# Performance work log

Hardware: AMD Instinct MI355X
Metric: run time of the kernel (lower is better)

The kernel has to match this reference:

```python
import jax, jax.numpy as jnp
import numpy as np

S = 41          # seq_len
D_IN = 1280
D_OUT = 1024
HEADS = 4
HC = D_OUT // HEADS
EPS = 1e-5

# ---- static edge construction (faithful to the torch code, incl. duplicate edges) ----

def _local_edges(s, window=1):
    e = []
    for i in range(s):
        for j in range(max(0, i - window), min(s, i + window + 1)):
            if i != j:
                e += [(i, j), (j, i)]
    return np.array(e, dtype=np.int32).T

def _region_edges(s):
    e = []
    step = s // 3
    for st in range(0, s, step):
        blk = range(st, min(st + step, s))
        for i in blk:
            for j in blk:
                if i != j:
                    e += [(i, j), (j, i)]
    return np.array(e, dtype=np.int32).T

def _global_edges(s):
    r, c = np.triu_indices(s, 1)  # torch.combinations: (i, j) with i < j
    return np.stack([r, c]).astype(np.int32)

def _batch_edges(e, b, s):
    off = np.arange(b, dtype=np.int32) * s
    return (e[:, None, :] + off[None, :, None]).reshape(2, -1)

_LOCAL = _local_edges(S)
_REGION = _region_edges(S)
_GLOBAL = _global_edges(S)

# ---- layer primitives ----

def _layernorm(x, g, b):
    mu = x.mean(-1, keepdims=True)
    v = ((x - mu) ** 2).mean(-1, keepdims=True)
    return (x - mu) / jnp.sqrt(v + EPS) * g + b

def _gcn(x, w, b, src, tgt, n):
    # PyG GCNConv: x' = D^-1/2 (A + I) D^-1/2 (x W) + b
    h = x @ w
    sl = jnp.arange(n, dtype=src.dtype)
    s = jnp.concatenate([src, sl]); t = jnp.concatenate([tgt, sl])
    deg = jax.ops.segment_sum(jnp.ones(t.shape, h.dtype), t, n)
    dinv = jnp.where(deg > 0, jax.lax.rsqrt(jnp.maximum(deg, 1.0)), 0.0)
    norm = dinv[s] * dinv[t]
    return jax.ops.segment_sum(h[s] * norm[:, None], t, n) + b

def _gat(x, w, a_src, a_dst, b, src, tgt, n):
    # PyG GATConv (shared lin, self loops, leaky_relu 0.2, softmax over incoming edges)
    h = (x @ w).reshape(n, HEADS, HC)
    sl = jnp.arange(n, dtype=src.dtype)
    s = jnp.concatenate([src, sl]); t = jnp.concatenate([tgt, sl])
    al_s = (h * a_src).sum(-1)  # [n, H]
    al_d = (h * a_dst).sum(-1)
    e = jax.nn.leaky_relu(al_s[s] + al_d[t], 0.2)  # [E, H]
    m = jax.ops.segment_max(e, t, n)
    ex = jnp.exp(e - m[t])
    den = jax.ops.segment_sum(ex, t, n)
    alpha = ex / den[t]
    out = jax.ops.segment_sum(h[s] * alpha[:, :, None], t, n)
    return out.reshape(n, HEADS * HC) + b

def _sage(x, wl, bl, wr, src, tgt, n):
    # PyG SAGEConv: mean-aggregate neighbors, plus root transform
    cnt = jax.ops.segment_sum(jnp.ones(src.shape, x.dtype), tgt, n)
    agg = jax.ops.segment_sum(x[src], tgt, n) / jnp.maximum(cnt, 1.0)[:, None]
    return agg @ wl + bl + x @ wr


def setup_inputs() -> dict:
    key = jax.random.key(0)
    ks = jax.random.split(key, 16)
    sc = 0.02
    f32 = jnp.float32
    inp = {
        'x': jax.random.normal(ks[0], (512, S, D_IN), f32),
        'att_w': jax.random.normal(ks[1], (D_IN, 1), f32) * sc,
        'att_b': jnp.zeros((1,), f32),
        'gcn_w': jax.random.normal(ks[2], (D_IN, D_OUT), f32) * sc,
        'gcn_b': jnp.zeros((D_OUT,), f32),
        'sn_g': jnp.ones((D_OUT,), f32), 'sn_b': jnp.zeros((D_OUT,), f32),
        'gat_w': jax.random.normal(ks[3], (D_IN, D_OUT), f32) * sc,
        'gat_as': jax.random.normal(ks[4], (HEADS, HC), f32) * sc,
        'gat_ad': jax.random.normal(ks[5], (HEADS, HC), f32) * sc,
        'gat_b': jnp.zeros((D_OUT,), f32),
        'mn_g': jnp.ones((D_OUT,), f32), 'mn_b': jnp.zeros((D_OUT,), f32),
        'sage_wl': jax.random.normal(ks[6], (D_IN, D_OUT), f32) * sc,
        'sage_bl': jnp.zeros((D_OUT,), f32),
        'sage_wr': jax.random.normal(ks[7], (D_IN, D_OUT), f32) * sc,
        'fp_w1': jax.random.normal(ks[8], (D_IN, 512), f32) * sc,
        'fp_b1': jnp.zeros((512,), f32),
        'fp_w2': jax.random.normal(ks[9], (512, S), f32) * sc,
        'fp_b2': jnp.zeros((S,), f32),
        'dn_g': jnp.ones((D_OUT,), f32), 'dn_b': jnp.zeros((D_OUT,), f32),
        'gate_w': jax.random.normal(ks[10], (3 * D_OUT, 3), f32) * sc,
        'gate_b': jnp.zeros((3,), f32),
    }
    return inp


def reference(x, att_w, att_b, gcn_w, gcn_b, sn_g, sn_b, gat_w, gat_as, gat_ad, gat_b,
              mn_g, mn_b, sage_wl, sage_bl, sage_wr, fp_w1, fp_b1, fp_w2, fp_b2,
              dn_g, dn_b, gate_w, gate_b):
    B = x.shape[0]
    N = B * S
    le = jnp.asarray(_batch_edges(_LOCAL, B, S))
    re = jnp.asarray(_batch_edges(_REGION, B, S))
    ge = jnp.asarray(_batch_edges(_GLOBAL, B, S))

    xf = x.reshape(N, D_IN)
    # shallow: local gating -> GCN -> LN
    enhanced = xf * jax.nn.sigmoid(xf @ att_w + att_b)
    shallow = _gcn(enhanced, gcn_w, gcn_b, le[0], le[1], N)
    shallow = _layernorm(shallow.reshape(B, S, D_OUT), sn_g, sn_b)
    # medium: GAT over region blocks -> LN
    gat = _gat(xf, gat_w, gat_as[None], gat_ad[None], gat_b, re[0], re[1], N)
    gat = _layernorm(gat.reshape(B, S, D_OUT), mn_g, mn_b)
    # deep: learned propagation mixing, SAGE over global edges -> LN
    pw = jax.nn.softmax(jax.nn.relu(x @ fp_w1 + fp_b1) @ fp_w2 + fp_b2, axis=-1)  # [B,S,S]
    sage_in = jnp.einsum('bij,bjd->bid', pw, x).reshape(N, D_IN)
    sage = _sage(sage_in, sage_wl, sage_bl, sage_wr, ge[0], ge[1], N)
    sage = _layernorm(sage.reshape(B, S, D_OUT), dn_g, dn_b)
    # gated branch mixing
    combined = jnp.concatenate([shallow, gat, sage], axis=-1)
    gates = jax.nn.softmax(combined @ gate_w + gate_b, axis=-1)
    total = gates[..., 0:1] * shallow + gates[..., 1:2] * gat + gates[..., 2:3] * sage
    return (shallow, gat, total)
```

## Files before the change

### kernel.cpp

```cpp
#include <hip/hip_runtime.h>
#include <math.h>

static constexpr int S    = 41;
static constexpr int DIN  = 1280;
static constexpr int DOUT = 1024;
static constexpr int HEADS = 4;
static constexpr int HC   = 256;

typedef __attribute__((ext_vector_type(4))) float f32x4;
typedef __attribute__((ext_vector_type(8))) short short8;

__device__ __forceinline__ ushort f2bf(float f) {
  uint u = __float_as_uint(f);
  uint r = u + 0x7fffu + ((u >> 16) & 1u);
  return (ushort)(r >> 16);
}
__device__ __forceinline__ float bf2f(ushort u) {
  return __uint_as_float(((uint)u) << 16);
}

__device__ __forceinline__ void gload16(const ushort* g, ushort* l) {
  __builtin_amdgcn_global_load_lds((const __attribute__((address_space(1))) void*)g,
                                   (__attribute__((address_space(3))) void*)l, 16, 0, 0);
}


__device__ __forceinline__ float warpReduceSum(float v) {
#pragma unroll
  for (int off = 32; off; off >>= 1) v += __shfl_down(v, off);
  return v;
}

__device__ __forceinline__ void blockReduce6(float* v) {
  __shared__ float red6[6][4];
  int w = threadIdx.x >> 6, lane = threadIdx.x & 63;
#pragma unroll
  for (int r = 0; r < 6; ++r) v[r] = warpReduceSum(v[r]);
  __syncthreads();
  if (lane == 0) {
#pragma unroll
    for (int r = 0; r < 6; ++r) red6[r][w] = v[r];
  }
  __syncthreads();
#pragma unroll
  for (int r = 0; r < 6; ++r)
    v[r] = red6[r][0] + red6[r][1] + red6[r][2] + red6[r][3];
}

__device__ __forceinline__ void blockReduce3v(float* v) {
  __shared__ float red3[3][4];
  int w = threadIdx.x >> 6, lane = threadIdx.x & 63;
#pragma unroll
  for (int r = 0; r < 3; ++r) v[r] = warpReduceSum(v[r]);
  __syncthreads();
  if (lane == 0) {
#pragma unroll
    for (int r = 0; r < 3; ++r) red3[r][w] = v[r];
  }
  __syncthreads();
#pragma unroll
  for (int r = 0; r < 3; ++r)
    v[r] = red3[r][0] + red3[r][1] + red3[r][2] + red3[r][3];
}


__global__ __launch_bounds__(256) void cvtsig_kernel(
    const float4* __restrict__ x, const float* __restrict__ att_w,
    const float* __restrict__ att_b, ushort4* __restrict__ xb, float* __restrict__ sig)
{
  int row  = blockIdx.x * 4 + (threadIdx.x >> 6);
  int lane = threadIdx.x & 63;
  const float4* xr = x + (size_t)row * (DIN / 4);
  const float4* wr = (const float4*)att_w;
  ushort4* xo = xb + (size_t)row * (DIN / 4);
  float acc = 0.f;
#pragma unroll
  for (int k = 0; k < DIN / 4 / 64; ++k) {
    float4 a = xr[lane + k * 64];
    float4 w = wr[lane + k * 64];
    acc += a.x * w.x + a.y * w.y + a.z * w.z + a.w * w.w;
    ushort4 o;
    o.x = f2bf(a.x); o.y = f2bf(a.y); o.z = f2bf(a.z); o.w = f2bf(a.w);
    xo[lane + k * 64] = o;
  }
  acc = warpReduceSum(acc);
  if (lane == 0) sig[row] = 1.f / (1.f + expf(-(acc + att_b[0])));
}


__global__ __launch_bounds__(256) void wcvt_kernel(const float* __restrict__ W,
                                                   ushort* __restrict__ out,
                                                   int K, int N, int ostride, int koff) {
  __shared__ float t[32][33];
  int n0 = blockIdx.x * 32, k0 = blockIdx.y * 32;
  int tx = threadIdx.x & 31, ty = threadIdx.x >> 5;
#pragma unroll
  for (int r = 0; r < 4; ++r) {
    int k = ty + r * 8;
    t[k][tx] = W[(size_t)(k0 + k) * N + n0 + tx];
  }
  __syncthreads();
#pragma unroll
  for (int r = 0; r < 4; ++r) {
    int nn = ty + r * 8;
    out[(size_t)(n0 + nn) * ostride + koff + k0 + tx] = f2bf(t[tx][nn]);
  }
}

__global__ __launch_bounds__(256) void w2cvt_kernel(const float* __restrict__ w2,
                                                    ushort* __restrict__ wpw) {
  int idx = blockIdx.x * 256 + threadIdx.x;
  int n = idx >> 9, k = idx & 511;
  wpw[idx] = (n < S) ? f2bf(w2[(size_t)k * S + n]) : (ushort)0;
}


struct Epi {
  void* dst[5];
  const float* bias[5];
  int nend[5];
  int ld[5];
  int relu[5];
  const float* rs;
};


__global__ __launch_bounds__(512, 1) void gemm256(
    const ushort* __restrict__ A, const ushort* __restrict__ Bt, int K, int nb, Epi e)
{
  __shared__ __align__(16) ushort As[3][256 * 32];
  __shared__ __align__(16) ushort Bs[3][256 * 32];

  const int bid = blockIdx.x;
  const int bm  = (bid / nb) * 256;
  const int bn  = (bid % nb) * 256;

  const int tid  = threadIdx.x;
  const int w    = tid >> 6;
  const int lane = tid & 63;
  const int l16  = lane & 15;
  const int l4   = lane >> 4;
  const int wr   = w >> 2;
  const int wc   = w & 3;
  const int m0   = wr * 128;
  const int n0   = wc * 64;

  const int rloc = lane >> 2;
  const int cpos = lane & 3;
  const int cdat = (cpos - (rloc >> 1)) & 3;
  const int srow = w * 32 + rloc;
  const int scol = cdat * 8;

  f32x4 acc[8][4];
#pragma unroll
  for (int i = 0; i < 8; ++i)
#pragma unroll
    for (int j = 0; j < 4; ++j) acc[i][j] = (f32x4)0.f;

  const ushort* pA0 = A  + (size_t)(bm + srow) * K + scol;
  const ushort* pA1 = A  + (size_t)(bm + srow + 16) * K + scol;
  const ushort* pB0 = Bt + (size_t)(bn + srow) * K + scol;
  const ushort* pB1 = Bt + (size_t)(bn + srow + 16) * K + scol;

  auto stage = [&](int buf, int kt) {
    gload16(pA0 + kt, &As[buf][w * 1024]);
    gload16(pA1 + kt, &As[buf][w * 1024 + 512]);
    gload16(pB0 + kt, &Bs[buf][w * 1024]);
    gload16(pB1 + kt, &Bs[buf][w * 1024 + 512]);
  };

  const int rchunk = ((l4 + (l16 >> 1)) & 3) * 8;

  const int nsteps = K >> 5;
  stage(0, 0); stage(1, 32); stage(2, 64);

  for (int t = 0; t < nsteps; ++t) {
    if (t == 0)                asm volatile("s_waitcnt vmcnt(8)" ::: "memory");
    else if (t == nsteps - 1)  asm volatile("s_waitcnt vmcnt(0)" ::: "memory");
    else                       asm volatile("s_waitcnt vmcnt(4)" ::: "memory");
    __builtin_amdgcn_s_barrier();
    asm volatile("" ::: "memory");

    if (t >= 1 && t + 2 < nsteps) stage((t + 2) % 3, (t + 2) * 32);

    const int cur = t % 3;
    short8 a[8], b[4];
#pragma unroll
    for (int i = 0; i < 8; ++i)
      a[i] = *reinterpret_cast<const short8*>(&As[cur][(m0 + i * 16 + l16) * 32 + rchunk]);
#pragma unroll
    for (int j = 0; j < 4; ++j)
      b[j] = *reinterpret_cast<const short8*>(&Bs[cur][(n0 + j * 16 + l16) * 32 + rchunk]);
    __builtin_amdgcn_s_setprio(1);
#pragma unroll
    for (int i = 0; i < 8; ++i)
#pragma unroll
      for (int j = 0; j < 4; ++j)
        acc[i][j] = __builtin_amdgcn_mfma_f32_16x16x32_bf16(a[i], b[j], acc[i][j], 0, 0, 0);
    __builtin_amdgcn_s_setprio(0);
  }

  void* dstv; const float* bias; const float* rs = nullptr; int ldc, cb, relu;
  if (bn < e.nend[0])      { dstv = e.dst[0]; ldc = e.ld[0]; cb = bn;             bias = e.bias[0]; relu = e.relu[0]; rs = e.rs; }
  else if (bn < e.nend[1]) { dstv = e.dst[1]; ldc = e.ld[1]; cb = bn - e.nend[0]; bias = e.bias[1]; relu = e.relu[1]; }
  else if (bn < e.nend[2]) { dstv = e.dst[2]; ldc = e.ld[2]; cb = bn - e.nend[1]; bias = e.bias[2]; relu = e.relu[2]; }
  else if (bn < e.nend[3]) { dstv = e.dst[3]; ldc = e.ld[3]; cb = bn - e.nend[2]; bias = e.bias[3]; relu = e.relu[3]; }
  else                     { dstv = e.dst[4]; ldc = e.ld[4]; cb = bn - e.nend[3]; bias = e.bias[4]; relu = e.relu[4]; }

#pragma unroll
  for (int i = 0; i < 8; ++i) {
    int mbase = bm + m0 + i * 16 + l4 * 4;
    float rsv[4];
#pragma unroll
    for (int r = 0; r < 4; ++r) rsv[r] = rs ? rs[mbase + r] : 1.f;
#pragma unroll
    for (int j = 0; j < 4; ++j) {
      int col = cb + n0 + j * 16 + l16;
      float bv = bias ? bias[col] : 0.f;
#pragma unroll
      for (int r = 0; r < 4; ++r) {
        float t = acc[i][j][r] * rsv[r] + bv;
        if (relu) t = fmaxf(t, 0.f);
        ((ushort*)dstv)[(size_t)(mbase + r) * ldc + col] = f2bf(t);
      }
    }
  }
}


template<bool F32OUT>
__global__ __launch_bounds__(256) void gemm_bf16(
    const ushort* __restrict__ A, const ushort* __restrict__ Bt, int K, int nb, Epi e)
{
  __shared__ __align__(16) ushort As[3][128 * 32];
  __shared__ __align__(16) ushort Bs[3][128 * 32];

  const int bid = blockIdx.x;
  const int bm  = (bid / nb) * 128;
  const int bn  = (bid % nb) * 128;

  const int tid  = threadIdx.x;
  const int w    = tid >> 6;
  const int lane = tid & 63;
  const int l16  = lane & 15;
  const int l4   = lane >> 4;
  const int m0   = (w >> 1) * 64;
  const int n0   = (w & 1) * 64;

  const int rloc = lane >> 2;
  const int cpos = lane & 3;
  const int cdat = (cpos - (rloc >> 1)) & 3;
  const int srow = w * 32 + rloc;
  const int scol = cdat * 8;

  f32x4 acc[4][4];
#pragma unroll
  for (int i = 0; i < 4; ++i)
#pragma unroll
    for (int j = 0; j < 4; ++j) acc[i][j] = (f32x4)0.f;

  const ushort* pA0 = A  + (size_t)(bm + srow) * K + scol;
  const ushort* pA1 = A  + (size_t)(bm + srow + 16) * K + scol;
  const ushort* pB0 = Bt + (size_t)(bn + srow) * K + scol;
  const ushort* pB1 = Bt + (size_t)(bn + srow + 16) * K + scol;

  auto stage = [&](int buf, int kt) {
    gload16(pA0 + kt, &As[buf][w * 1024]);
    gload16(pA1 + kt, &As[buf][w * 1024 + 512]);
    gload16(pB0 + kt, &Bs[buf][w * 1024]);
    gload16(pB1 + kt, &Bs[buf][w * 1024 + 512]);
  };

  const int rchunk = ((l4 + (l16 >> 1)) & 3) * 8;

  const int nsteps = K >> 5;
  stage(0, 0); stage(1, 32); stage(2, 64);

  for (int t = 0; t < nsteps; ++t) {
    if (t == 0)                asm volatile("s_waitcnt vmcnt(8)" ::: "memory");
    else if (t == nsteps - 1)  asm volatile("s_waitcnt vmcnt(0)" ::: "memory");
    else                       asm volatile("s_waitcnt vmcnt(4)" ::: "memory");
    __builtin_amdgcn_s_barrier();
    asm volatile("" ::: "memory");

    if (t >= 1 && t + 2 < nsteps) stage((t + 2) % 3, (t + 2) * 32);

    const int cur = t % 3;
    short8 a[4], b[4];
#pragma unroll
    for (int i = 0; i < 4; ++i)
      a[i] = *reinterpret_cast<const short8*>(&As[cur][(m0 + i * 16 + l16) * 32 + rchunk]);
#pragma unroll
    for (int j = 0; j < 4; ++j)
      b[j] = *reinterpret_cast<const short8*>(&Bs[cur][(n0 + j * 16 + l16) * 32 + rchunk]);
    __builtin_amdgcn_s_setprio(1);
#pragma unroll
    for (int i = 0; i < 4; ++i)
#pragma unroll
      for (int j = 0; j < 4; ++j)
        acc[i][j] = __builtin_amdgcn_mfma_f32_16x16x32_bf16(a[i], b[j], acc[i][j], 0, 0, 0);
    __builtin_amdgcn_s_setprio(0);
  }

  void* dstv; const float* bias; const float* rs = nullptr; int ldc, cb, relu;
  if (bn < e.nend[0])      { dstv = e.dst[0]; ldc = e.ld[0]; cb = bn;             bias = e.bias[0]; relu = e.relu[0]; rs = e.rs; }
  else if (bn < e.nend[1]) { dstv = e.dst[1]; ldc = e.ld[1]; cb = bn - e.nend[0]; bias = e.bias[1]; relu = e.relu[1]; }
  else if (bn < e.nend[2]) { dstv = e.dst[2]; ldc = e.ld[2]; cb = bn - e.nend[1]; bias = e.bias[2]; relu = e.relu[2]; }
  else if (bn < e.nend[3]) { dstv = e.dst[3]; ldc = e.ld[3]; cb = bn - e.nend[2]; bias = e.bias[3]; relu = e.relu[3]; }
  else                     { dstv = e.dst[4]; ldc = e.ld[4]; cb = bn - e.nend[3]; bias = e.bias[4]; relu = e.relu[4]; }

#pragma unroll
  for (int i = 0; i < 4; ++i) {
    int mbase = bm + m0 + i * 16 + l4 * 4;
    float rsv[4];
#pragma unroll
    for (int r = 0; r < 4; ++r) rsv[r] = rs ? rs[mbase + r] : 1.f;
#pragma unroll
    for (int j = 0; j < 4; ++j) {
      int col = cb + n0 + j * 16 + l16;
      float bv = bias ? bias[col] : 0.f;
#pragma unroll
      for (int r = 0; r < 4; ++r) {
        float t = acc[i][j][r] * rsv[r] + bv;
        if (relu) t = fmaxf(t, 0.f);
        if (F32OUT) ((float*)dstv)[(size_t)(mbase + r) * ldc + col] = t;
        else        ((ushort*)dstv)[(size_t)(mbase + r) * ldc + col] = f2bf(t);
      }
    }
  }
}


__global__ __launch_bounds__(256) void pwprep_kernel(
    const float* __restrict__ fp2, const float* __restrict__ fp_b2,
    float* __restrict__ pc)
{
  int b = blockIdx.x;
  int tid = threadIdx.x, wv = tid >> 6, lane = tid & 63;
  __shared__ float pws[S][S];
  for (int i = wv; i < S; i += 4) {
    float v = (lane < S) ? (fp2[(size_t)(b * S + i) * 128 + lane] + fp_b2[lane]) : -1e30f;
    float m = v;
#pragma unroll
    for (int off = 32; off; off >>= 1) m = fmaxf(m, __shfl_xor(m, off));
    float e = (lane < S) ? expf(v - m) : 0.f;
    float sum = e;
#pragma unroll
    for (int off = 32; off; off >>= 1) sum += __shfl_xor(sum, off);
    if (lane < S) {
      float p = e / sum;
      pws[i][lane] = p;
      pc[((size_t)b * S + i) * 128 + lane] = p;
    }
  }
  __syncthreads();
  if (tid < S) {
    float run = 0.f;
    for (int i = 0; i < S; ++i) {
      pc[((size_t)b * S + i) * 128 + 64 + tid] = (i > 0) ? run / (float)i : 0.f;
      run += pws[i][tid];
    }
  }
}


__global__ __launch_bounds__(256) void mixc_kernel(
    const float* __restrict__ pc, const ushort* __restrict__ xr,
    const ushort* __restrict__ xl, const float* __restrict__ sage_bl,
    ushort* __restrict__ hbuf)
{
  int b  = blockIdx.y;
  int d0 = blockIdx.x * 256;
  int tid = threadIdx.x;

  float xrv[S], xlv[S];
  const ushort* xrp = xr + (size_t)(b * S) * DOUT + d0 + tid;
  const ushort* xlp = xl + (size_t)(b * S) * DOUT + d0 + tid;
#pragma unroll
  for (int j = 0; j < S; ++j) {
    xrv[j] = bf2f(xrp[(size_t)j * DOUT]);
    xlv[j] = bf2f(xlp[(size_t)j * DOUT]);
  }
  float bl = sage_bl[d0 + tid];
  ushort* op = hbuf + (size_t)(b * S) * DOUT + d0 + tid;
  const float* pcb = pc + (size_t)(b * S) * 128;
  for (int i = 0; i < S; ++i) {
    const float* row = pcb + (size_t)i * 128;
    float acc = bl;
#pragma unroll
    for (int j = 0; j < S; ++j)
      acc += row[j] * xrv[j] + row[64 + j] * xlv[j];
    op[(size_t)i * DOUT] = f2bf(acc);
  }
}


__device__ __forceinline__ float dinv_local(int j) {
  return rsqrtf((j == 0 || j == S - 1) ? 3.f : 5.f);
}

__global__ __launch_bounds__(256) void tail_fused(
    const ushort* __restrict__ gcnh, const ushort* __restrict__ Cgat,
    const ushort* __restrict__ hbuf,
    const float* __restrict__ gcn_b, const float* __restrict__ sn_g, const float* __restrict__ sn_b,
    const float* __restrict__ gat_as, const float* __restrict__ gat_ad, const float* __restrict__ gat_b,
    const float* __restrict__ mn_g, const float* __restrict__ mn_b,
    const float* __restrict__ dn_g, const float* __restrict__ dn_b,
    const float* __restrict__ gw, const float* __restrict__ gb,
    float* __restrict__ out, int N)
{
  int b  = blockIdx.x >> 2;
  int rb = blockIdx.x & 3;
  int lo = rb * 13;
  int cnt = (rb < 3) ? 13 : 2;
  size_t OUT = (size_t)N * DOUT;
  int tid = threadIdx.x;
  int wv = tid >> 6, lane = tid & 63;
  int d0 = tid * 4;
  int head = tid >> 6;

  __shared__ __align__(16) ushort hs[13][DOUT];
  __shared__ float alpha[13][13][HEADS];
  __shared__ float als_l[13][HEADS], ald_l[13][HEADS];

  for (int r = 0; r < cnt; ++r) {
    const ushort4* src = (const ushort4*)(Cgat + (size_t)(b * S + lo + r) * DOUT);
    ((ushort4*)hs[r])[tid] = src[tid];
  }
  __syncthreads();

  {
    const float4* a4 = (const float4*)(gat_as + wv * HC);
    const float4* d4 = (const float4*)(gat_ad + wv * HC);
    float4 av = a4[lane], dv = d4[lane];
    for (int s = 0; s < cnt; ++s) {
      ushort4 hv4 = ((const ushort4*)&hs[s][wv * HC])[lane];
      float h0 = bf2f(hv4.x), h1 = bf2f(hv4.y), h2 = bf2f(hv4.z), h3 = bf2f(hv4.w);
      float a = h0 * av.x + h1 * av.y + h2 * av.z + h3 * av.w;
      float d = h0 * dv.x + h1 * dv.y + h2 * dv.z + h3 * dv.w;
      a = warpReduceSum(a);
      d = warpReduceSum(d);
      if (lane == 0) { als_l[s][wv] = a; ald_l[s][wv] = d; }
    }
  }
  __syncthreads();

  if (tid < cnt * HEADS) {
    int t = tid >> 2, hd = tid & 3;
    float myald = ald_l[t][hd];
    float m = -1e30f;
    for (int s = 0; s < cnt; ++s) {
      float v = als_l[s][hd] + myald;
      v = (v > 0.f) ? v : 0.2f * v;
      m = fmaxf(m, v);
    }
    float den = 0.f;
    for (int s = 0; s < cnt; ++s) {
      float v = als_l[s][hd] + myald;
      v = (v > 0.f) ? v : 0.2f * v;
      float ev = expf(v - m) * ((s == t) ? 1.f : 2.f);
      alpha[t][s][hd] = ev;
      den += ev;
    }
    float inv = 1.f / den;
    for (int s = 0; s < cnt; ++s) alpha[t][s][hd] *= inv;
  }
  __syncthreads();

  float4 gcnb4 = *(const float4*)(gcn_b + d0);
  float4 sng4  = *(const float4*)(sn_g + d0);
  float4 snb4  = *(const float4*)(sn_b + d0);
  float4 gatb4 = *(const float4*)(gat_b + d0);
  float4 mng4  = *(const float4*)(mn_g + d0);
  float4 mnb4  = *(const float4*)(mn_b + d0);
  float4 dng4  = *(const float4*)(dn_g + d0);
  float4 dnb4  = *(const float4*)(dn_b + d0);
  float gwsh[4][3], gwga[4][3], gwsa[4][3];
#pragma unroll
  for (int q = 0; q < 4; ++q)
#pragma unroll
    for (int c = 0; c < 3; ++c) {
      gwsh[q][c] = gw[(size_t)(d0 + q) * 3 + c];
      gwga[q][c] = gw[(size_t)(DOUT + d0 + q) * 3 + c];
      gwsa[q][c] = gw[(size_t)(2 * DOUT + d0 + q) * 3 + c];
    }

  for (int t = 0; t < cnt; ++t) {
    int i = lo + t;
    size_t n = (size_t)(b * S + i);

    float di = dinv_local(i);
    float wc = di * di;
    float wl = (i > 0)     ? 2.f * di * dinv_local(i - 1) : 0.f;
    float wr = (i < S - 1) ? 2.f * di * dinv_local(i + 1) : 0.f;
    const ushort* hc = gcnh + n * DOUT + d0;
    ushort4 c4  = *(const ushort4*)hc;
    ushort4 lft = (i > 0)     ? *(const ushort4*)(hc - DOUT) : ushort4{0, 0, 0, 0};
    ushort4 rgt = (i < S - 1) ? *(const ushort4*)(hc + DOUT) : ushort4{0, 0, 0, 0};
    const ushort* cp = (const ushort*)&c4;
    const ushort* lp = (const ushort*)&lft;
    const ushort* rp = (const ushort*)&rgt;
    const float* gbp = (const float*)&gcnb4;
    float sh[4];
#pragma unroll
    for (int q = 0; q < 4; ++q)
      sh[q] = wc * bf2f(cp[q]) + wl * bf2f(lp[q]) + wr * bf2f(rp[q]) + gbp[q];

    float ga[4] = {0.f, 0.f, 0.f, 0.f};
    for (int si = 0; si < cnt; ++si) {
      float aj = alpha[t][si][head];
      ushort4 hv = *(const ushort4*)&hs[si][d0];
      ga[0] += aj * bf2f(hv.x);
      ga[1] += aj * bf2f(hv.y);
      ga[2] += aj * bf2f(hv.z);
      ga[3] += aj * bf2f(hv.w);
    }
    const float* gab = (const float*)&gatb4;
#pragma unroll
    for (int q = 0; q < 4; ++q) ga[q] += gab[q];

    ushort4 s4v = *(const ushort4*)(hbuf + n * DOUT + d0);
    const ushort* sp = (const ushort*)&s4v;
    float sa[4];
#pragma unroll
    for (int q = 0; q < 4; ++q) sa[q] = bf2f(sp[q]);

    float red[6] = {0.f, 0.f, 0.f, 0.f, 0.f, 0.f};
#pragma unroll
    for (int q = 0; q < 4; ++q) {
      red[0] += sh[q]; red[1] += sh[q] * sh[q];
      red[2] += ga[q]; red[3] += ga[q] * ga[q];
      red[4] += sa[q]; red[5] += sa[q] * sa[q];
    }
    blockReduce6(red);
    float mu0 = red[0] * (1.f / DOUT), r0 = rsqrtf(red[1] * (1.f / DOUT) - mu0 * mu0 + 1e-5f);
    float mu1 = red[2] * (1.f / DOUT), r1 = rsqrtf(red[3] * (1.f / DOUT) - mu1 * mu1 + 1e-5f);
    float mu2 = red[4] * (1.f / DOUT), r2 = rsqrtf(red[5] * (1.f / DOUT) - mu2 * mu2 + 1e-5f);

    const float* sngp = (const float*)&sng4; const float* snbp = (const float*)&snb4;
    const float* mngp = (const float*)&mng4; const float* mnbp = (const float*)&mnb4;
    const float* dngp = (const float*)&dng4; const float* dnbp = (const float*)&dnb4;
    float shn[4], gan[4], san[4];
#pragma unroll
    for (int q = 0; q < 4; ++q) {
      shn[q] = (sh[q] - mu0) * r0 * sngp[q] + snbp[q];
      gan[q] = (ga[q] - mu1) * r1 * mngp[q] + mnbp[q];
      san[q] = (sa[q] - mu2) * r2 * dngp[q] + dnbp[q];
    }

    float p[3] = {0.f, 0.f, 0.f};
#pragma unroll
    for (int q = 0; q < 4; ++q) {
#pragma unroll
      for (int c = 0; c < 3; ++c)
        p[c] += shn[q] * gwsh[q][c] + gan[q] * gwga[q][c] + san[q] * gwsa[q][c];
    }
    blockReduce3v(p);
    float l0 = p[0] + gb[0], l1 = p[1] + gb[1], l2 = p[2] + gb[2];
    float m = fmaxf(l0, fmaxf(l1, l2));
    float e0 = expf(l0 - m), e1 = expf(l1 - m), e2 = expf(l2 - m);
    float inv = 1.f / (e0 + e1 + e2);
    float g0 = e0 * inv, g1 = e1 * inv, g2 = e2 * inv;

    float4 o0, o1, o2;
    float* o0p = (float*)&o0; float* o1p = (float*)&o1; float* o2p = (float*)&o2;
#pragma unroll
    for (int q = 0; q < 4; ++q) {
      o0p[q] = shn[q];
      o1p[q] = gan[q];
      o2p[q] = g0 * shn[q] + g1 * gan[q] + g2 * san[q];
    }
    *(float4*)(out + n * DOUT + d0)           = o0;
    *(float4*)(out + OUT + n * DOUT + d0)     = o1;
    *(float4*)(out + 2 * OUT + n * DOUT + d0) = o2;
  }
}


extern "C" void kernel_launch(void* const* d_in, const int* in_sizes, int n_in,
                              void* d_out, int out_size, void* d_ws, size_t ws_size,
                              hipStream_t stream) {
  const float* x       = (const float*)d_in[0];
  const float* att_w   = (const float*)d_in[1];
  const float* att_b   = (const float*)d_in[2];
  const float* gcn_w   = (const float*)d_in[3];
  const float* gcn_b   = (const float*)d_in[4];
  const float* sn_g    = (const float*)d_in[5];
  const float* sn_b    = (const float*)d_in[6];
  const float* gat_w   = (const float*)d_in[7];
  const float* gat_as  = (const float*)d_in[8];
  const float* gat_ad  = (const float*)d_in[9];
  const float* gat_b   = (const float*)d_in[10];
  const float* mn_g    = (const float*)d_in[11];
  const float* mn_b    = (const float*)d_in[12];
  const float* sage_wl = (const float*)d_in[13];
  const float* sage_bl = (const float*)d_in[14];
  const float* sage_wr = (const float*)d_in[15];
  const float* fp_w1   = (const float*)d_in[16];
  const float* fp_b1   = (const float*)d_in[17];
  const float* fp_w2   = (const float*)d_in[18];
  const float* fp_b2   = (const float*)d_in[19];
  const float* dn_g    = (const float*)d_in[20];
  const float* dn_b    = (const float*)d_in[21];
  const float* gate_w  = (const float*)d_in[22];
  const float* gate_b  = (const float*)d_in[23];

  const int B = in_sizes[0] / (S * DIN);
  const int N = B * S;
  const int MB  = N / 128;
  const int MB2 = N / 256;
  const int NMEGA = 4608;
  float* out = (float*)d_out;

  char* ws = (char*)d_ws;
  size_t off = 0;
  auto alloc = [&](size_t bytes) { size_t p = off; off += (bytes + 255) & ~(size_t)255; return p; };
  ushort* xb   = (ushort*)(ws + alloc((size_t)N * DIN * 2));
  ushort* Bt   = (ushort*)(ws + alloc((size_t)NMEGA * DIN * 2));
  ushort* wpw  = (ushort*)(ws + alloc((size_t)128 * 512 * 2));
  ushort* gcnh = (ushort*)(ws + alloc((size_t)N * DOUT * 2));
  ushort* Cgat = (ushort*)(ws + alloc((size_t)N * DOUT * 2));
  ushort* xr   = (ushort*)(ws + alloc((size_t)N * DOUT * 2));
  ushort* xl   = (ushort*)(ws + alloc((size_t)N * DOUT * 2));
  ushort* hbuf = (ushort*)(ws + alloc((size_t)N * DOUT * 2));
  float*  fp2  = (float*)(ws + alloc((size_t)N * 128 * 4));
  float*  pc   = (float*)(ws + alloc((size_t)N * 128 * 4));
  float*  sig  = (float*)(ws + alloc((size_t)N * 4));
  ushort* fp1  = hbuf;

  dim3 blk(256);

  cvtsig_kernel<<<N / 4, blk, 0, stream>>>((const float4*)x, att_w, att_b, (ushort4*)xb, sig);
  wcvt_kernel<<<dim3(DOUT / 32, DIN / 32), blk, 0, stream>>>(gcn_w, Bt, DIN, DOUT, DIN, 0);
  wcvt_kernel<<<dim3(DOUT / 32, DIN / 32), blk, 0, stream>>>(gat_w, Bt + (size_t)1024 * DIN, DIN, DOUT, DIN, 0);
  wcvt_kernel<<<dim3(512 / 32, DIN / 32), blk, 0, stream>>>(fp_w1, Bt + (size_t)2048 * DIN, DIN, 512, DIN, 0);
  wcvt_kernel<<<dim3(DOUT / 32, DIN / 32), blk, 0, stream>>>(sage_wr, Bt + (size_t)2560 * DIN, DIN, DOUT, DIN, 0);
  wcvt_kernel<<<dim3(DOUT / 32, DIN / 32), blk, 0, stream>>>(sage_wl, Bt + (size_t)3584 * DIN, DIN, DOUT, DIN, 0);
  w2cvt_kernel<<<dim3(128 * 512 / 256), blk, 0, stream>>>(fp_w2, wpw);

  Epi e1;
  e1.dst[0] = gcnh; e1.dst[1] = Cgat; e1.dst[2] = fp1; e1.dst[3] = xr; e1.dst[4] = xl;
  e1.bias[0] = nullptr; e1.bias[1] = nullptr; e1.bias[2] = fp_b1; e1.bias[3] = nullptr; e1.bias[4] = nullptr;
  e1.nend[0] = 1024; e1.nend[1] = 2048; e1.nend[2] = 2560; e1.nend[3] = 3584; e1.nend[4] = 4608;
  e1.ld[0] = DOUT; e1.ld[1] = DOUT; e1.ld[2] = 512; e1.ld[3] = DOUT; e1.ld[4] = DOUT;
  e1.relu[0] = 0; e1.relu[1] = 0; e1.relu[2] = 1; e1.relu[3] = 0; e1.relu[4] = 0;
  e1.rs = sig;
  gemm256<<<dim3(MB2 * (NMEGA / 256)), dim3(512), 0, stream>>>(xb, Bt, DIN, NMEGA / 256, e1);

  Epi epw;
  epw.dst[0] = fp2; epw.dst[1] = nullptr; epw.dst[2] = nullptr; epw.dst[3] = nullptr; epw.dst[4] = nullptr;
  epw.bias[0] = nullptr; epw.bias[1] = nullptr; epw.bias[2] = nullptr; epw.bias[3] = nullptr; epw.bias[4] = nullptr;
  epw.nend[0] = 1 << 30; epw.nend[1] = 1 << 30; epw.nend[2] = 1 << 30; epw.nend[3] = 1 << 30; epw.nend[4] = 1 << 30;
  epw.ld[0] = 128; epw.ld[1] = 128; epw.ld[2] = 128; epw.ld[3] = 128; epw.ld[4] = 128;
  epw.relu[0] = 0; epw.relu[1] = 0; epw.relu[2] = 0; epw.relu[3] = 0; epw.relu[4] = 0;
  epw.rs = nullptr;
  gemm_bf16<true><<<dim3(MB), blk, 0, stream>>>(fp1, wpw, 512, 1, epw);

  pwprep_kernel<<<B, blk, 0, stream>>>(fp2, fp_b2, pc);
  mixc_kernel<<<dim3(DOUT / 256, B), blk, 0, stream>>>(pc, xr, xl, sage_bl, hbuf);

  tail_fused<<<B * 4, blk, 0, stream>>>(gcnh, Cgat, hbuf,
                                        gcn_b, sn_g, sn_b,
                                        gat_as, gat_ad, gat_b,
                                        mn_g, mn_b, dn_g, dn_b,
                                        gate_w, gate_b, out, N);
}
```

Measured before the change: 700.7 us.

## Restructure mega GEMM into 8-phase pipeline with split A/B staging

Replaces the 3-buffer 32-wide K-step GEMM with a 4-buffer scheme. Each iteration processes two 32-wide K halves (64 total) and splits each half into two M sub-phases with barriers between them. A and B tile loads are issued separately across phases, so global-to-LDS traffic interleaves more finely with MFMA work and register pressure for A fragments drops from 8 to 4. It adds more barriers per K step, and correctness depends on the vmcnt accounting and buffer reuse ordering being right.

```diff
diff --git a/kernel.cpp b/kernel.cpp
--- a/kernel.cpp
+++ b/kernel.cpp
@@ -125,31 +125,41 @@
 };
 
 
-__global__ __launch_bounds__(512, 1) void gemm256(
+__global__ __launch_bounds__(512, 1) void gemm8p(
     const ushort* __restrict__ A, const ushort* __restrict__ Bt, int K, int nb, Epi e)
 {
-  __shared__ __align__(16) ushort As[3][256 * 32];
-  __shared__ __align__(16) ushort Bs[3][256 * 32];
+  __shared__ __align__(16) ushort As[4 * 8192];
+  __shared__ __align__(16) ushort Bs[4 * 8192];
 
   const int bid = blockIdx.x;
   const int bm  = (bid / nb) * 256;
   const int bn  = (bid % nb) * 256;
 
   const int tid  = threadIdx.x;
-  const int w    = tid >> 6;
+  const int wv   = tid >> 6;
   const int lane = tid & 63;
   const int l16  = lane & 15;
   const int l4   = lane >> 4;
-  const int wr   = w >> 2;
-  const int wc   = w & 3;
-  const int m0   = wr * 128;
-  const int n0   = wc * 64;
-
-  const int rloc = lane >> 2;
-  const int cpos = lane & 3;
-  const int cdat = (cpos - (rloc >> 1)) & 3;
-  const int srow = w * 32 + rloc;
-  const int scol = cdat * 8;
+  const int m0   = (wv >> 2) * 128;
+  const int n0   = (wv & 3) * 64;
+
+  const int rd0 = wv * 16 + (lane >> 2);
+  const int rd1 = 128 + wv * 16 + (lane >> 2);
+  const int cs0 = ((lane & 3) - ((rd0 >> 1) & 3)) & 3;
+  const int cs1 = ((lane & 3) - ((rd1 >> 1) & 3)) & 3;
+
+  auto stageA = [&](int h, int Tt) {
+    int kof = Tt * 64 + (h & 1) * 32;
+    gload16(A + (size_t)(bm + rd0) * K + kof + cs0 * 8, &As[h * 8192 + wv * 512]);
+    gload16(A + (size_t)(bm + rd1) * K + kof + cs1 * 8, &As[h * 8192 + (8 + wv) * 512]);
+  };
+  auto stageB = [&](int h, int Tt) {
+    int kof = Tt * 64 + (h & 1) * 32;
+    gload16(Bt + (size_t)(bn + rd0) * K + kof + cs0 * 8, &Bs[h * 8192 + wv * 512]);
+    gload16(Bt + (size_t)(bn + rd1) * K + kof + cs1 * 8, &Bs[h * 8192 + (8 + wv) * 512]);
+  };
+
+  const int rchunk = ((l4 + ((l16 >> 1) & 3)) & 3) * 8;
 
   f32x4 acc[8][4];
 #pragma unroll
@@ -157,46 +167,82 @@
 #pragma unroll
     for (int j = 0; j < 4; ++j) acc[i][j] = (f32x4)0.f;
 
-  const ushort* pA0 = A  + (size_t)(bm + srow) * K + scol;
-  const ushort* pA1 = A  + (size_t)(bm + srow + 16) * K + scol;
-  const ushort* pB0 = Bt + (size_t)(bn + srow) * K + scol;
-  const ushort* pB1 = Bt + (size_t)(bn + srow + 16) * K + scol;
-
-  auto stage = [&](int buf, int kt) {
-    gload16(pA0 + kt, &As[buf][w * 1024]);
-    gload16(pA1 + kt, &As[buf][w * 1024 + 512]);
-    gload16(pB0 + kt, &Bs[buf][w * 1024]);
-    gload16(pB1 + kt, &Bs[buf][w * 1024 + 512]);
-  };
-
-  const int rchunk = ((l4 + (l16 >> 1)) & 3) * 8;
-
-  const int nsteps = K >> 5;
-  stage(0, 0); stage(1, 32); stage(2, 64);
-
-  for (int t = 0; t < nsteps; ++t) {
-    if (t == 0)                asm volatile("s_waitcnt vmcnt(8)" ::: "memory");
-    else if (t == nsteps - 1)  asm volatile("s_waitcnt vmcnt(0)" ::: "memory");
-    else                       asm volatile("s_waitcnt vmcnt(4)" ::: "memory");
+  const int NT = K >> 6;
+
+  stageA(0, 0); stageB(0, 0);
+  stageA(1, 0); stageB(1, 0);
+  stageA(2, 1); stageB(2, 1);
+
+  for (int T = 0; T < NT; ++T) {
+    const int db = T & 1;
+    const int hA = db * 2;
+    const int hB = db * 2 + 1;
+    short8 a[4], b[4];
+
+    if (T + 1 < NT) asm volatile("s_waitcnt vmcnt(8)" ::: "memory");
+    else            asm volatile("s_waitcnt vmcnt(4)" ::: "memory");
     __builtin_amdgcn_s_barrier();
     asm volatile("" ::: "memory");
-
-    if (t >= 1 && t + 2 < nsteps) stage((t + 2) % 3, (t + 2) * 32);
-
-    const int cur = t % 3;
-    short8 a[8], b[4];
-#pragma unroll
-    for (int i = 0; i < 8; ++i)
-      a[i] = *reinterpret_cast<const short8*>(&As[cur][(m0 + i * 16 + l16) * 32 + rchunk]);
+    if (T + 1 < NT) stageA((db ^ 1) * 2 + 1, T + 1);
+#pragma unroll
+    for (int i = 0; i < 4; ++i)
+      a[i] = *reinterpret_cast<const short8*>(&As[hA * 8192 + (m0 + i * 16 + l16) * 32 + rchunk]);
 #pragma unroll
     for (int j = 0; j < 4; ++j)
-      b[j] = *reinterpret_cast<const short8*>(&Bs[cur][(n0 + j * 16 + l16) * 32 + rchunk]);
+      b[j] = *reinterpret_cast<const short8*>(&Bs[hA * 8192 + (n0 + j * 16 + l16) * 32 + rchunk]);
     __builtin_amdgcn_s_setprio(1);
 #pragma unroll
-    for (int i = 0; i < 8; ++i)
+    for (int i = 0; i < 4; ++i)
 #pragma unroll
       for (int j = 0; j < 4; ++j)
         acc[i][j] = __builtin_amdgcn_mfma_f32_16x16x32_bf16(a[i], b[j], acc[i][j], 0, 0, 0);
+    __builtin_amdgcn_s_setprio(0);
+
+    __builtin_amdgcn_s_barrier();
+    asm volatile("" ::: "memory");
+    if (T + 1 < NT) stageB((db ^ 1) * 2 + 1, T + 1);
+#pragma unroll
+    for (int i = 0; i < 4; ++i)
+      a[i] = *reinterpret_cast<const short8*>(&As[hA * 8192 + (m0 + 64 + i * 16 + l16) * 32 + rchunk]);
+    __builtin_amdgcn_s_setprio(1);
+#pragma unroll
+    for (int i = 0; i < 4; ++i)
+#pragma unroll
+      for (int j = 0; j < 4; ++j)
+        acc[4 + i][j] = __builtin_amdgcn_mfma_f32_16x16x32_bf16(a[i], b[j], acc[4 + i][j], 0, 0, 0);
+    __builtin_amdgcn_s_setprio(0);
+
+    if (T + 1 < NT) asm volatile("s_waitcnt vmcnt(8)" ::: "memory");
+    else            asm volatile("s_waitcnt vmcnt(0)" ::: "memory");
+    __builtin_amdgcn_s_barrier();
+    asm volatile("" ::: "memory");
+    if (T + 2 < NT) stageA(db * 2, T + 2);
+#pragma unroll
+    for (int i = 0; i < 4; ++i)
+      a[i] = *reinterpret_cast<const short8*>(&As[hB * 8192 + (m0 + i * 16 + l16) * 32 + rchunk]);
+#pragma unroll
+    for (int j = 0; j < 4; ++j)
+      b[j] = *reinterpret_cast<const short8*>(&Bs[hB * 8192 + (n0 + j * 16 + l16) * 32 + rchunk]);
+    __builtin_amdgcn_s_setprio(1);
+#pragma unroll
+    for (int i = 0; i < 4; ++i)
+#pragma unroll
+      for (int j = 0; j < 4; ++j)
+        acc[i][j] = __builtin_amdgcn_mfma_f32_16x16x32_bf16(a[i], b[j], acc[i][j], 0, 0, 0);
+    __builtin_amdgcn_s_setprio(0);
+
+    __builtin_amdgcn_s_barrier();
+    asm volatile("" ::: "memory");
+    if (T + 2 < NT) stageB(db * 2, T + 2);
+#pragma unroll
+    for (int i = 0; i < 4; ++i)
+      a[i] = *reinterpret_cast<const short8*>(&As[hB * 8192 + (m0 + 64 + i * 16 + l16) * 32 + rchunk]);
+    __builtin_amdgcn_s_setprio(1);
+#pragma unroll
+    for (int i = 0; i < 4; ++i)
+#pragma unroll
+      for (int j = 0; j < 4; ++j)
+        acc[4 + i][j] = __builtin_amdgcn_mfma_f32_16x16x32_bf16(a[i], b[j], acc[4 + i][j], 0, 0, 0);
     __builtin_amdgcn_s_setprio(0);
   }
 
@@ -645,7 +691,7 @@
   e1.ld[0] = DOUT; e1.ld[1] = DOUT; e1.ld[2] = 512; e1.ld[3] = DOUT; e1.ld[4] = DOUT;
   e1.relu[0] = 0; e1.relu[1] = 0; e1.relu[2] = 1; e1.relu[3] = 0; e1.relu[4] = 0;
   e1.rs = sig;
-  gemm256<<<dim3(MB2 * (NMEGA / 256)), dim3(512), 0, stream>>>(xb, Bt, DIN, NMEGA / 256, e1);
+  gemm8p<<<dim3(MB2 * (NMEGA / 256)), dim3(512), 0, stream>>>(xb, Bt, DIN, NMEGA / 256, e1);
 
   Epi epw;
   epw.dst[0] = fp2; epw.dst[1] = nullptr; epw.dst[2] = nullptr; epw.dst[3] = nullptr; epw.dst[4] = nullptr;
```

Result: no change. 693.2 us (-1.1%).
